# Optimization experiments

Hardware: AMD Instinct MI355X
Metric: run time of the kernel (lower is better)

Reference implementation:

```python
import jax, jax.numpy as jnp
import numpy as np

ALPHA = 0.0005
TAU = 0.2


def setup_inputs() -> dict:
    key = jax.random.key(0)
    k1, k2, k3 = jax.random.split(key, 3)
    x_batch = jax.random.normal(k1, (2048, 4096), dtype=jnp.float32)
    y_batch = jax.random.normal(k2, (2048, 4096), dtype=jnp.float32)
    # conv weight [out_ch, in_ch, kh, kw]; sliced along dim 2 (F = 64)
    conv_w = jax.random.normal(k3, (512, 512, 64, 3), dtype=jnp.float32) * 0.05
    return {"x_batch": x_batch, "y_batch": y_batch, "conv_w": conv_w}


def _diversity_reg(conv_w, tau):
    # slices conv_w[:, :, i, :] flattened -> rows of v: [F, out*in*kw]
    F = conv_w.shape[2]
    v = jnp.transpose(conv_w, (2, 0, 1, 3)).reshape(F, -1)
    norms = jnp.sqrt(jnp.sum(v * v, axis=1))  # [F]
    gram = v @ v.T  # [F, F] -- memory-bound tall-skinny reduction
    sim = gram / (norms[:, None] * norms[None, :])
    eye = jnp.eye(F, dtype=bool)
    # keep iff tau < sim <= 1 and i != j; zeroed entries are detached (constant 0)
    mask = (sim > tau) & (sim <= 1.0) & (~eye)
    return jnp.sum(jnp.where(mask, sim, 0.0))


def reference(x_batch, y_batch, conv_w):
    # loss_function = MSELoss (mean reduction)
    loss_value = jnp.mean((x_batch - y_batch) ** 2)
    reg_value = _diversity_reg(conv_w, TAU)
    return loss_value + ALPHA * reg_value
```

## Files before the change

kernel.cpp:

```cpp
#include <hip/hip_runtime.h>

typedef __attribute__((ext_vector_type(8)))  short   short8;
typedef __attribute__((ext_vector_type(4)))  unsigned uint4v;
typedef __attribute__((ext_vector_type(16))) float   f32x16;

constexpr int GRAM_BLOCKS = 384;
constexpr int MSE_BLOCKS  = 128;
constexpr int BLOCK       = 256;
constexpr int SLAB_F      = 192;
constexpr int CHUNK_F     = 3072;
constexpr int NCHUNK      = 16384;
constexpr int GRAM_WAVES  = GRAM_BLOCKS * 4;
constexpr int NSLICE      = 8;
constexpr unsigned MSE_N4 = 2097152u;
constexpr int MSE_THREADS = MSE_BLOCKS * BLOCK;


struct F3 { float v[3]; };
struct Chunk { F3 a0[4], a1[4], b0[4], b1[4]; };

__device__ __forceinline__ unsigned pk_bf16(float a, float b) {
  unsigned a2 = __builtin_bit_cast(unsigned, a) + 0x8000u;
  unsigned b2 = __builtin_bit_cast(unsigned, b) + 0x8000u;
  return __builtin_amdgcn_perm(b2, a2, 0x07060302u);
}

__device__ __forceinline__ void load_chunk(const float* __restrict__ W, int c,
                                           int laneoff, Chunk& ch) {
  const float* s = W + (size_t)c * CHUNK_F + laneoff;
#pragma unroll
  for (int bp = 0; bp < 4; ++bp) {
    const float* p = s + bp * 384;
    ch.a0[bp] = *(const F3*)(p);
    ch.a1[bp] = *(const F3*)(p + 96);
    ch.b0[bp] = *(const F3*)(p + 192);
    ch.b1[bp] = *(const F3*)(p + 288);
  }
}

__device__ __forceinline__ void mac_chunk(const Chunk& c, f32x16& a00, f32x16& a01,
                                          f32x16& a11) {
#pragma unroll
  for (int k = 0; k < 3; ++k) {
    unsigned fl[4], fh[4];
#pragma unroll
    for (int bp = 0; bp < 4; ++bp) {
      fl[bp] = pk_bf16(c.a0[bp].v[k], c.b0[bp].v[k]);
      fh[bp] = pk_bf16(c.a1[bp].v[k], c.b1[bp].v[k]);
    }
    uint4v vl = {fl[0], fl[1], fl[2], fl[3]};
    uint4v vh = {fh[0], fh[1], fh[2], fh[3]};
    short8 lo = __builtin_bit_cast(short8, vl);
    short8 hv = __builtin_bit_cast(short8, vh);
    a00 = __builtin_amdgcn_mfma_f32_32x32x16_bf16(lo, lo, a00, 0, 0, 0);
    a01 = __builtin_amdgcn_mfma_f32_32x32x16_bf16(lo, hv, a01, 0, 0, 0);
    a11 = __builtin_amdgcn_mfma_f32_32x32x16_bf16(hv, hv, a11, 0, 0, 0);
  }
}

__global__ __launch_bounds__(BLOCK, 2) void k_main(
    const float* __restrict__ X, const float* __restrict__ Y,
    const float* __restrict__ W, float* __restrict__ ws) {
  __shared__ float red[2][3072];
  const int bid = blockIdx.x;
  const int tid = threadIdx.x;
  const int wave = tid >> 6;
  const int lane = tid & 63;

  if (bid >= GRAM_BLOCKS) {
    const unsigned t0 = (unsigned)((bid - GRAM_BLOCKS) * BLOCK + tid);
    const float4* x4 = (const float4*)X;
    const float4* y4 = (const float4*)Y;
    float acc = 0.f;
#pragma unroll 8
    for (int it = 0; it < 64; ++it) {
      unsigned i = t0 + (unsigned)it * (unsigned)MSE_THREADS;
      float4 a = x4[i], b = y4[i];
      float d0 = a.x - b.x, d1 = a.y - b.y, d2 = a.z - b.z, d3 = a.w - b.w;
      acc += d0 * d0 + d1 * d1 + d2 * d2 + d3 * d3;
    }
#pragma unroll
    for (int o = 32; o; o >>= 1) acc += __shfl_xor(acc, o, 64);
    __shared__ float wsum[4];
    if (lane == 0) wsum[wave] = acc;
    __syncthreads();
    if (tid == 0) ws[bid - GRAM_BLOCKS] = wsum[0] + wsum[1] + wsum[2] + wsum[3];
    return;
  }

  const int r    = lane & 31;
  const int hi   = lane >> 5;
  const int laneoff = hi * 1536 + 3 * r;
  const int wg = bid * 4 + wave;

  f32x16 a00{}, a01{}, a11{};
  Chunk ca, cb;
  int c = wg;
  load_chunk(W, c, laneoff, ca);
  c += GRAM_WAVES;
  for (;;) {
    if (c < NCHUNK) load_chunk(W, c, laneoff, cb);
    mac_chunk(ca, a00, a01, a11);
    if (c >= NCHUNK) break;
    c += GRAM_WAVES;
    if (c < NCHUNK) load_chunk(W, c, laneoff, ca);
    mac_chunk(cb, a00, a01, a11);
    if (c >= NCHUNK) break;
    c += GRAM_WAVES;
  }

  if (wave < 2) {
#pragma unroll
    for (int rg = 0; rg < 16; ++rg) {
      red[wave][       rg * 64 + lane] = a00[rg];
      red[wave][1024 + rg * 64 + lane] = a01[rg];
      red[wave][2048 + rg * 64 + lane] = a11[rg];
    }
  }
  __syncthreads();
  if (wave >= 2) {
    float* dst = red[wave - 2];
#pragma unroll
    for (int rg = 0; rg < 16; ++rg) {
      dst[       rg * 64 + lane] += a00[rg];
      dst[1024 + rg * 64 + lane] += a01[rg];
      dst[2048 + rg * 64 + lane] += a11[rg];
    }
  }
  __syncthreads();
  float* slice = ws + 128 + (bid & (NSLICE - 1)) * 3072;
  for (int e = tid; e < 3072; e += BLOCK)
    atomicAdd(&slice[e], red[0][e] + red[1][e]);
}

__global__ __launch_bounds__(256) void k_fin(const float* __restrict__ ws,
                                             float* __restrict__ out) {
  __shared__ float g[3072];
  __shared__ float n2[64];
  __shared__ float wsum[4];
  __shared__ float msum_s[4];
  const int tid = threadIdx.x;
  const int wave = tid >> 6, lane = tid & 63;

  for (int e = tid; e < 3072; e += 256) {
    float s = 0.f;
#pragma unroll
    for (int sl = 0; sl < NSLICE; ++sl) s += ws[128 + sl * 3072 + e];
    g[e] = s;
  }
  float m = (tid < 128) ? ws[tid] : 0.f;
#pragma unroll
  for (int o = 32; o; o >>= 1) m += __shfl_xor(m, o, 64);
  if (lane == 0) msum_s[wave] = m;
  __syncthreads();

  for (int e = tid; e < 3072; e += 256) {
    int tl = e >> 10, rg = (e >> 6) & 15, l = e & 63;
    int il = (rg & 3) + 8 * (rg >> 2) + 4 * (l >> 5);
    int jl = l & 31;
    if (tl != 1 && il == jl) n2[il + (tl == 2 ? 32 : 0)] = g[e];
  }
  __syncthreads();

  float local = 0.f;
  for (int e = tid; e < 3072; e += 256) {
    int tl = e >> 10, rg = (e >> 6) & 15, l = e & 63;
    int il = (rg & 3) + 8 * (rg >> 2) + 4 * (l >> 5);
    int jl = l & 31;
    int i, j; float wgt;
    if (tl == 0)      { i = il;      j = jl;      wgt = 1.f; }
    else if (tl == 1) { i = il;      j = jl + 32; wgt = 2.f; }
    else              { i = il + 32; j = jl + 32; wgt = 1.f; }
    if (i != j) {
      float sim = g[e] / sqrtf(n2[i] * n2[j]);
      if (sim > 0.2f && sim <= 1.0f) local += wgt * sim;
    }
  }
#pragma unroll
  for (int o = 32; o; o >>= 1) local += __shfl_xor(local, o, 64);
  if (lane == 0) wsum[wave] = local;
  __syncthreads();
  if (tid == 0) {
    float reg_sum = wsum[0] + wsum[1] + wsum[2] + wsum[3];
    float mse_sum = msum_s[0] + msum_s[1] + msum_s[2] + msum_s[3];
    out[0] = mse_sum * (1.0f / 8388608.0f) + 0.0005f * reg_sum;
  }
}

extern "C" void kernel_launch(void* const* d_in, const int* in_sizes, int n_in,
                              void* d_out, int out_size, void* d_ws, size_t ws_size,
                              hipStream_t stream) {
  const float* X = (const float*)d_in[0];
  const float* Y = (const float*)d_in[1];
  const float* W = (const float*)d_in[2];
  float* ws = (float*)d_ws;

  hipMemsetAsync((void*)((char*)d_ws + 128 * sizeof(float)), 0,
                 NSLICE * 3072 * sizeof(float), stream);
  k_main<<<GRAM_BLOCKS + MSE_BLOCKS, BLOCK, 0, stream>>>(X, Y, W, ws);
  k_fin<<<1, 256, 0, stream>>>(ws, (float*)d_out);
}
```

Measured before the change: 65.24 us.

## Replace atomic slice reduction with per-block partials and multi-block flag reduction

Each gram block now writes its 3072-float partial Gram directly to its own workspace slot, with vectorized stores, instead of atomically adding into 8 shared slices. This removes the memset launch and the atomic contention. A second kernel with 96 blocks sums the 384 partials column-wise and publishes them with release flags, and block 0 spins on the flags before doing the final similarity and MSE combine. The MSE loads also become nontemporal. In exchange it adds about 4.7 MB of partial-buffer traffic and relies on all reducer blocks being co-resident so the spin-wait cannot deadlock.

```diff
diff --git a/kernel.cpp b/kernel.cpp
--- a/kernel.cpp
+++ b/kernel.cpp
@@ -3,18 +3,21 @@
 typedef __attribute__((ext_vector_type(8)))  short   short8;
 typedef __attribute__((ext_vector_type(4)))  unsigned uint4v;
 typedef __attribute__((ext_vector_type(16))) float   f32x16;
+typedef __attribute__((ext_vector_type(4)))  float   f4;
 
 constexpr int GRAM_BLOCKS = 384;
 constexpr int MSE_BLOCKS  = 128;
 constexpr int BLOCK       = 256;
-constexpr int SLAB_F      = 192;
 constexpr int CHUNK_F     = 3072;
 constexpr int NCHUNK      = 16384;
 constexpr int GRAM_WAVES  = GRAM_BLOCKS * 4;
-constexpr int NSLICE      = 8;
-constexpr unsigned MSE_N4 = 2097152u;
 constexpr int MSE_THREADS = MSE_BLOCKS * BLOCK;
-
+constexpr int RED_BLOCKS  = 96;
+
+constexpr int MSE_OFF  = 0;
+constexpr int FLAG_OFF = 128;
+constexpr int GF_OFF   = 256;
+constexpr int PART_OFF = 4096;
 
 struct F3 { float v[3]; };
 struct Chunk { F3 a0[4], a1[4], b0[4], b1[4]; };
@@ -58,10 +61,10 @@
   }
 }
 
-__global__ __launch_bounds__(BLOCK, 2) void k_main(
+__global__ __launch_bounds__(BLOCK, 2) void k_a(
     const float* __restrict__ X, const float* __restrict__ Y,
     const float* __restrict__ W, float* __restrict__ ws) {
-  __shared__ float red[2][3072];
+  __shared__ __align__(16) float red[2][3072];
   const int bid = blockIdx.x;
   const int tid = threadIdx.x;
   const int wave = tid >> 6;
@@ -69,14 +72,15 @@
 
   if (bid >= GRAM_BLOCKS) {
     const unsigned t0 = (unsigned)((bid - GRAM_BLOCKS) * BLOCK + tid);
-    const float4* x4 = (const float4*)X;
-    const float4* y4 = (const float4*)Y;
+    const f4* x4 = (const f4*)X;
+    const f4* y4 = (const f4*)Y;
     float acc = 0.f;
 #pragma unroll 8
     for (int it = 0; it < 64; ++it) {
       unsigned i = t0 + (unsigned)it * (unsigned)MSE_THREADS;
-      float4 a = x4[i], b = y4[i];
-      float d0 = a.x - b.x, d1 = a.y - b.y, d2 = a.z - b.z, d3 = a.w - b.w;
+      f4 a = __builtin_nontemporal_load(x4 + i);
+      f4 b = __builtin_nontemporal_load(y4 + i);
+      float d0 = a[0] - b[0], d1 = a[1] - b[1], d2 = a[2] - b[2], d3 = a[3] - b[3];
       acc += d0 * d0 + d1 * d1 + d2 * d2 + d3 * d3;
     }
 #pragma unroll
@@ -84,7 +88,7 @@
     __shared__ float wsum[4];
     if (lane == 0) wsum[wave] = acc;
     __syncthreads();
-    if (tid == 0) ws[bid - GRAM_BLOCKS] = wsum[0] + wsum[1] + wsum[2] + wsum[3];
+    if (tid == 0) ws[MSE_OFF + bid - GRAM_BLOCKS] = wsum[0] + wsum[1] + wsum[2] + wsum[3];
     return;
   }
 
@@ -128,31 +132,62 @@
     }
   }
   __syncthreads();
-  float* slice = ws + 128 + (bid & (NSLICE - 1)) * 3072;
-  for (int e = tid; e < 3072; e += BLOCK)
-    atomicAdd(&slice[e], red[0][e] + red[1][e]);
-}
-
-__global__ __launch_bounds__(256) void k_fin(const float* __restrict__ ws,
-                                             float* __restrict__ out) {
+  const f4* r0 = (const f4*)&red[0][0];
+  const f4* r1 = (const f4*)&red[1][0];
+  f4* p4 = (f4*)(ws + PART_OFF + (size_t)bid * 3072);
+#pragma unroll
+  for (int q = tid; q < 768; q += BLOCK) {
+    f4 a = r0[q], b = r1[q];
+    p4[q] = a + b;
+  }
+}
+
+__global__ __launch_bounds__(256) void k_b(float* __restrict__ ws,
+                                           float* __restrict__ out) {
+  __shared__ float r2[4][32];
   __shared__ float g[3072];
   __shared__ float n2[64];
+  __shared__ float msum_s[4];
   __shared__ float wsum[4];
-  __shared__ float msum_s[4];
   const int tid = threadIdx.x;
-  const int wave = tid >> 6, lane = tid & 63;
-
-  for (int e = tid; e < 3072; e += 256) {
-    float s = 0.f;
-#pragma unroll
-    for (int sl = 0; sl < NSLICE; ++sl) s += ws[128 + sl * 3072 + e];
-    g[e] = s;
-  }
-  float m = (tid < 128) ? ws[tid] : 0.f;
+  const int lane = tid & 63, wv = tid >> 6, el = lane & 31, ph = lane >> 5;
+  const int b = blockIdx.x;
+  const int w0 = b * 32;
+  int* flags = (int*)(ws + FLAG_OFF);
+
+  const float* base = ws + PART_OFF + (size_t)(ph + 2 * wv) * 3072 + w0 + el;
+  float acc = 0.f;
+#pragma unroll 8
+  for (int i = 0; i < 48; ++i) acc += base[(size_t)i * 24576];
+  acc += __shfl_xor(acc, 32, 64);
+  if (ph == 0) r2[wv][el] = acc;
+  __syncthreads();
+  if (tid < 32)
+    ws[GF_OFF + w0 + tid] = r2[0][tid] + r2[1][tid] + r2[2][tid] + r2[3][tid];
+  __syncthreads();
+  if (tid == 0) {
+    __threadfence();
+    __hip_atomic_store(&flags[b], 1, __ATOMIC_RELEASE, __HIP_MEMORY_SCOPE_AGENT);
+  }
+  if (b != 0) return;
+
+  if (tid < RED_BLOCKS) {
+    while (__hip_atomic_load(&flags[tid], __ATOMIC_RELAXED,
+                             __HIP_MEMORY_SCOPE_AGENT) != 1)
+      __builtin_amdgcn_s_sleep(8);
+  }
+  __syncthreads();
+  __threadfence();
+
+  for (int e = tid; e < 3072; e += 256) g[e] = ws[GF_OFF + e];
+
+  float m = (tid < 128) ? ws[MSE_OFF + tid] : 0.f;
 #pragma unroll
   for (int o = 32; o; o >>= 1) m += __shfl_xor(m, o, 64);
-  if (lane == 0) msum_s[wave] = m;
-  __syncthreads();
+  if (lane == 0) msum_s[wv] = m;
+  __syncthreads();
+
+  if (tid < RED_BLOCKS) flags[tid] = 0;
 
   for (int e = tid; e < 3072; e += 256) {
     int tl = e >> 10, rg = (e >> 6) & 15, l = e & 63;
@@ -178,7 +213,7 @@
   }
 #pragma unroll
   for (int o = 32; o; o >>= 1) local += __shfl_xor(local, o, 64);
-  if (lane == 0) wsum[wave] = local;
+  if (lane == 0) wsum[wv] = local;
   __syncthreads();
   if (tid == 0) {
     float reg_sum = wsum[0] + wsum[1] + wsum[2] + wsum[3];
@@ -195,8 +230,6 @@
   const float* W = (const float*)d_in[2];
   float* ws = (float*)d_ws;
 
-  hipMemsetAsync((void*)((char*)d_ws + 128 * sizeof(float)), 0,
-                 NSLICE * 3072 * sizeof(float), stream);
-  k_main<<<GRAM_BLOCKS + MSE_BLOCKS, BLOCK, 0, stream>>>(X, Y, W, ws);
-  k_fin<<<1, 256, 0, stream>>>(ws, (float*)d_out);
-}
+  k_a<<<GRAM_BLOCKS + MSE_BLOCKS, BLOCK, 0, stream>>>(X, Y, W, ws);
+  k_b<<<RED_BLOCKS, 256, 0, stream>>>(ws, (float*)d_out);
+}
```

Result: faster. 61.63 us (-5.5%).
